# Kernel optimization log

Measured on AMD Instinct MI355X. Metric: run time of the kernel, lower is better.

The kernel has to match this reference:

```python
import jax, jax.numpy as jnp
import numpy as np
from jax import lax

# dims (see shape_source)
B, C, H, W = 2, 128, 48, 48
HEADS = 4
G = 4                 # offset_groups = heads
DH = C // HEADS       # 32, dim_head
DF = 4                # downsample_factor
OKS = 6               # offset_kernel_size
PAD = (OKS - DF) // 2 # 1
OFFSET_SCALE = 4.0
CPB_DIM = C // 4      # 32
OD = C // G           # offset_dims = 32


def setup_inputs() -> dict:
    key = jax.random.key(0)
    ks = jax.random.split(key, 12)
    rn = lambda k, shape, s=0.05: jax.random.normal(k, shape, dtype=jnp.float32) * s
    return {
        "x": jax.random.normal(ks[0], (B, C, H, W), dtype=jnp.float32),
        "gamma": jax.random.normal(ks[1], (1,), dtype=jnp.float32),  # nn.Parameter([0.0]); randomized so both paths contribute
        "wq": rn(ks[2], (G, DH, C // G)),    # grouped 1x1 conv, groups=G
        "wk": rn(ks[3], (G, DH, C // G)),
        "wv": rn(ks[4], (G, DH, C // G)),
        "wo": rn(ks[5], (C, C)),             # to_out 1x1 conv
        "bo": jnp.zeros((C,), jnp.float32),
        "w_off_dw": rn(ks[6], (OD, 1, OKS, OKS)),  # depthwise conv k=6 s=4 p=1
        "b_off_dw": jnp.zeros((OD,), jnp.float32),
        "w_off_proj": rn(ks[7], (2, OD)),          # 1x1 conv to 2 offset channels, no bias
        "cpb_w0": rn(ks[8], (2, CPB_DIM), 0.5),
        "cpb_b0": jnp.zeros((CPB_DIM,), jnp.float32),
        "cpb_w1": rn(ks[9], (CPB_DIM, CPB_DIM), 0.2),
        "cpb_b1": jnp.zeros((CPB_DIM,), jnp.float32),
        "cpb_w2": rn(ks[10], (CPB_DIM, HEADS // G), 0.2),
        "cpb_b2": jnp.zeros((HEADS // G,), jnp.float32),
    }


def _bilinear_sample(img, px, py):
    """F.grid_sample(mode='bilinear', padding_mode='zeros') on pixel coords.
    img: (N, Cg, Hi, Wi); px, py: (N, Ho, Wo) -> (N, Cg, Ho, Wo)"""
    N, Cg, Hi, Wi = img.shape
    imgf = img.reshape(N, Cg, Hi * Wi)
    x0 = jnp.floor(px)
    y0 = jnp.floor(py)
    wx1 = px - x0
    wy1 = py - y0

    def corner(xc, yc, w):
        valid = (xc >= 0) & (xc <= Wi - 1) & (yc >= 0) & (yc <= Hi - 1)
        xi = jnp.clip(xc, 0, Wi - 1).astype(jnp.int32)
        yi = jnp.clip(yc, 0, Hi - 1).astype(jnp.int32)
        idx = (yi * Wi + xi).reshape(N, -1)
        vals = jnp.take_along_axis(imgf, idx[:, None, :], axis=2)  # (N,Cg,Ho*Wo)
        return vals * (w * valid).reshape(N, 1, -1)

    out = (corner(x0, y0, (1 - wx1) * (1 - wy1))
           + corner(x0 + 1, y0, wx1 * (1 - wy1))
           + corner(x0, y0 + 1, (1 - wx1) * wy1)
           + corner(x0 + 1, y0 + 1, wx1 * wy1))
    return out.reshape(N, Cg, px.shape[1], px.shape[2])


def _forward(x, gamma, wq, wk, wv, wo, bo, w_off_dw, b_off_dw, w_off_proj,
             cpb_w0, cpb_b0, cpb_w1, cpb_b1, cpb_w2, cpb_b2):
    b = x.shape[0]
    scale = DH ** -0.5
    xg = x.reshape(b, G, C // G, H, W)
    # grouped 1x1 conv -> queries (b, G, DH, H, W); channel layout (g d) == (h d) since G==HEADS
    q = jnp.einsum('bgchw,goc->bgohw', xg, wq)
    gq = q.reshape(b * G, DH, H, W)
    # to_offsets: depthwise conv (k=6, s=4, p=1) -> GELU -> 1x1 to 2ch -> tanh -> *offset_scale
    off = lax.conv_general_dilated(gq, w_off_dw, (DF, DF), [(PAD, PAD), (PAD, PAD)],
                                   feature_group_count=OD,
                                   dimension_numbers=('NCHW', 'OIHW', 'NCHW'))
    off = jax.nn.gelu(off + b_off_dw[None, :, None, None], approximate=False)
    off = jnp.tanh(jnp.einsum('bchw,oc->bohw', off, w_off_proj)) * OFFSET_SCALE  # (bG,2,Hd,Wd)
    Hd, Wd = off.shape[-2], off.shape[-1]
    gy, gx = jnp.meshgrid(jnp.arange(Hd, dtype=jnp.float32),
                          jnp.arange(Wd, dtype=jnp.float32), indexing='ij')
    vg0 = gx[None] + off[:, 0]  # channel 0 = x (meshgrid 'xy' in torch code)
    vg1 = gy[None] + off[:, 1]  # channel 1 = y
    vn0 = 2.0 * vg0 / max(Hd - 1, 1) - 1.0  # normalize_grid (H==W so h/w quirk is moot)
    vn1 = 2.0 * vg1 / max(Wd - 1, 1) - 1.0
    # grid_sample align_corners=False unnormalization: pix = ((u+1)*size - 1)/2
    px = ((vn0 + 1.0) * W - 1.0) / 2.0
    py = ((vn1 + 1.0) * H - 1.0) / 2.0
    kv = _bilinear_sample(xg.reshape(b * G, C // G, H, W), px, py)  # (bG, C/G, Hd, Wd)
    kvg = kv.reshape(b, G, C // G, Hd, Wd)
    k = jnp.einsum('bgchw,goc->bgohw', kvg, wk)
    v = jnp.einsum('bgchw,goc->bgohw', kvg, wv)
    i, j = H * W, Hd * Wd
    qh = q.reshape(b, HEADS, DH, i).transpose(0, 1, 3, 2) * scale  # (b,h,i,d)
    kh = k.reshape(b, HEADS, DH, j).transpose(0, 1, 3, 2)
    vh = v.reshape(b, HEADS, DH, j).transpose(0, 1, 3, 2)
    sim = jnp.einsum('bhid,bhjd->bhij', qh, kh)
    # CPB relative position bias
    gyq, gxq = jnp.meshgrid(jnp.arange(H, dtype=jnp.float32),
                            jnp.arange(W, dtype=jnp.float32), indexing='ij')
    qn0 = 2.0 * gxq / max(H - 1, 1) - 1.0
    qn1 = 2.0 * gyq / max(W - 1, 1) - 1.0
    grid_q = jnp.stack([qn0, qn1], -1).reshape(1, i, 1, 2)
    grid_kv = jnp.stack([vn0, vn1], -1).reshape(b * G, 1, j, 2)
    pos = grid_q - grid_kv                       # (bG, i, j, 2)
    bias = jnp.sign(pos) * jnp.log1p(jnp.abs(pos))
    h1 = jax.nn.relu(bias @ cpb_w0 + cpb_b0)
    h2 = jax.nn.relu(h1 @ cpb_w1 + cpb_b1)
    bias = h2 @ cpb_w2 + cpb_b2                  # (bG, i, j, heads//G)
    bias = bias.reshape(b, G, i, j, HEADS // G).transpose(0, 1, 4, 2, 3).reshape(b, HEADS, i, j)
    attn = jax.nn.softmax(sim + bias, axis=-1)
    outh = jnp.einsum('bhij,bhjd->bhid', attn, vh)
    out = outh.transpose(0, 1, 3, 2).reshape(b, C, H, W)  # 'b h (x y) d -> b (h d) x y'
    attention = jnp.einsum('bchw,oc->bohw', out, wo) + bo[None, :, None, None]
    return gamma[0] * attention + x, attention


def reference(x, gamma, wq, wk, wv, wo, bo, w_off_dw, b_off_dw, w_off_proj,
              cpb_w0, cpb_b0, cpb_w1, cpb_b1, cpb_w2, cpb_b2):
    return _forward(x, gamma, wq, wk, wv, wo, bo, w_off_dw, b_off_dw, w_off_proj,
                    cpb_w0, cpb_b0, cpb_w1, cpb_b1, cpb_w2, cpb_b2)
```

## Files before the change

kernel.cpp:

```cpp
#include <hip/hip_runtime.h>
#include <math.h>

#define HWHW 2304
#define JD   144
#define LSP  148

typedef __attribute__((ext_vector_type(8))) short short8;
typedef __attribute__((ext_vector_type(4))) float f32x4;

__device__ inline ushort f2bf(float f) {
  uint u = __float_as_uint(f);
  u += 0x7fffu + ((u >> 16) & 1u);
  return (ushort)(u >> 16);
}
__device__ inline float bf2f(ushort s) { return __uint_as_float((uint)s << 16); }
__device__ inline uint packbf(float hi, float lo) {
  return __builtin_amdgcn_perm(__float_as_uint(hi), __float_as_uint(lo), 0x07060302);
}


__global__ __launch_bounds__(256) void qproj_kernel(
    const float* __restrict__ x, const float* __restrict__ wq,
    ushort* __restrict__ qt) {
  int hw = blockIdx.x * 256 + threadIdx.x;
  int o0 = blockIdx.y * 8, bg = blockIdx.z;
  int b = bg >> 2, g = bg & 3;
  const float* xp = x + (b * 128 + g * 32) * HWHW + hw;
  float xv[32];
#pragma unroll
  for (int c = 0; c < 32; ++c) xv[c] = xp[c * HWHW];
  uint p[4];
#pragma unroll
  for (int oo = 0; oo < 8; oo += 2) {
    const float* w0r = wq + (g * 32 + o0 + oo) * 32;
    const float* w1r = wq + (g * 32 + o0 + oo + 1) * 32;
    float a0 = 0.f, a1 = 0.f;
#pragma unroll
    for (int c = 0; c < 32; ++c) { a0 += w0r[c] * xv[c]; a1 += w1r[c] * xv[c]; }
    p[oo >> 1] = (uint)f2bf(a0) | ((uint)f2bf(a1) << 16);
  }
  *(uint4*)(qt + ((long)bg * HWHW + hw) * 32 + o0) = make_uint4(p[0], p[1], p[2], p[3]);
}

__global__ __launch_bounds__(384) void offset_kv_kernel(
    const ushort* __restrict__ qt, const float* __restrict__ wdw,
    const float* __restrict__ bdw, const float* __restrict__ wproj,
    const float* __restrict__ x, const float* __restrict__ wk,
    const float* __restrict__ wv,
    float* __restrict__ vn0, float* __restrict__ vn1,
    ushort* __restrict__ ktb, ushort* __restrict__ vtb) {
  __shared__ float qs[288][32];
  __shared__ float wdws[36][32];
  __shared__ float wkl[32][33], wvl[32][33];
  __shared__ float kvs[32][13];
  __shared__ float spx[12], spy[12];
  int hd = blockIdx.x, bg = blockIdx.y, b = bg >> 2, g = bg & 3;
  int t = threadIdx.x;
  for (int u = t; u < 4608; u += 384) {
    int r = u >> 4, c2 = u & 15;
    int ry = r / 48, col = r - ry * 48;
    int hy = hd * 4 - 1 + ry;
    uint v = 0;
    if (hy >= 0 && hy < 48)
      v = ((const uint*)qt)[((long)bg * HWHW + hy * 48 + col) * 16 + c2];
    qs[r][c2 * 2] = bf2f((ushort)v);
    qs[r][c2 * 2 + 1] = bf2f((ushort)(v >> 16));
  }
  for (int u = t; u < 1152; u += 384) wdws[u >> 5][u & 31] = wdw[(u & 31) * 36 + (u >> 5)];
  for (int u = t; u < 1024; u += 384) {
    int d = u >> 5, c = u & 31;
    wkl[d][c] = wk[g * 1024 + u];
    wvl[d][c] = wv[g * 1024 + u];
  }
  __syncthreads();
  {
    int wd = t >> 5, c = t & 31;
    float s = 0.f;
#pragma unroll
    for (int ky = 0; ky < 6; ++ky) {
#pragma unroll
      for (int kx = 0; kx < 6; ++kx) {
        int wx = wd * 4 - 1 + kx;
        if (wx >= 0 && wx < 48)
          s += wdws[ky * 6 + kx][c] * qs[ky * 48 + wx][c];
      }
    }
    s += bdw[c];
    s = 0.5f * s * (1.f + erff(s * 0.70710678118654752f));
    float g0 = wproj[c] * s;
    float g1 = wproj[32 + c] * s;
#pragma unroll
    for (int k = 16; k >= 1; k >>= 1) {
      g0 += __shfl_xor(g0, k, 64);
      g1 += __shfl_xor(g1, k, 64);
    }
    if (c == 0) {
      float off0 = tanhf(g0) * 4.f;
      float off1 = tanhf(g1) * 4.f;
      float n0 = 2.f * ((float)wd + off0) / 11.f - 1.f;
      float n1 = 2.f * ((float)hd + off1) / 11.f - 1.f;
      int idx = bg * JD + hd * 12 + wd;
      vn0[idx] = n0;
      vn1[idx] = n1;
      spx[wd] = ((n0 + 1.f) * 48.f - 1.f) * 0.5f;
      spy[wd] = ((n1 + 1.f) * 48.f - 1.f) * 0.5f;
    }
  }
  __syncthreads();
  {
    int j = t >> 5, c = t & 31;
    float fx = spx[j], fy = spy[j];
    float x0 = floorf(fx), y0 = floorf(fy);
    float wx = fx - x0, wy = fy - y0;
    int xi = (int)x0, yi = (int)y0;
    const float* xp = x + (b * 128 + g * 32 + c) * HWHW;
    float v00 = 0.f, v10 = 0.f, v01 = 0.f, v11 = 0.f;
    bool okx0 = (xi >= 0) & (xi < 48), okx1 = (xi + 1 >= 0) & (xi + 1 < 48);
    if (yi >= 0 && yi < 48) {
      if (okx0) v00 = xp[yi * 48 + xi];
      if (okx1) v10 = xp[yi * 48 + xi + 1];
    }
    if (yi + 1 >= 0 && yi + 1 < 48) {
      if (okx0) v01 = xp[(yi + 1) * 48 + xi];
      if (okx1) v11 = xp[(yi + 1) * 48 + xi + 1];
    }
    kvs[c][j] = v00 * (1.f - wx) * (1.f - wy) + v10 * wx * (1.f - wy)
              + v01 * (1.f - wx) * wy + v11 * wx * wy;
  }
  __syncthreads();
  {
    int j = t >> 5, d = t & 31;
    float ak = 0.f, av = 0.f;
#pragma unroll
    for (int c = 0; c < 32; ++c) {
      float val = kvs[c][j];
      ak += wkl[d][c] * val;
      av += wvl[d][c] * val;
    }
    int jg = hd * 12 + j;
    ktb[bg * 4608 + jg * 32 + d] = f2bf(ak);
    vtb[bg * 5120 + d * 160 + jg] = f2bf(av);
  }
  if (hd == 0) {
    for (int u = t; u < 512; u += 384)
      vtb[bg * 5120 + (u >> 4) * 160 + 144 + (u & 15)] = 0;
  }
}

__global__ __launch_bounds__(256) void attn_fused_kernel(
    const ushort* __restrict__ qt, const ushort* __restrict__ ktb,
    const ushort* __restrict__ vtb,
    const float* __restrict__ vn0, const float* __restrict__ vn1,
    const float* __restrict__ w0, const float* __restrict__ b0,
    const float* __restrict__ w1, const float* __restrict__ b1,
    const float* __restrict__ w2, const float* __restrict__ b2,
    ushort* __restrict__ outh) {
  __shared__ __align__(16) char smem[10624];
  float* Ls = (float*)smem;
  float* sv0 = (float*)(smem + 9472);
  float* sv1 = (float*)(smem + 10048);

  int bg = blockIdx.y, b = bg >> 2, g = bg & 3;
  int i0 = blockIdx.x * 16;
  int t = threadIdx.x;
  int w = t >> 6, lane = t & 63;
  int lam = lane & 15, quad = lane >> 4;

  if (t < JD) { sv0[t] = vn0[bg * JD + t]; sv1[t] = vn1[bg * JD + t]; }

  float w00r[8], w01r[8], b0r[8];
#pragma unroll
  for (int j = 0; j < 8; ++j) {
    int k = quad * 8 + j;
    w00r[j] = w0[k]; w01r[j] = w0[32 + k]; b0r[j] = b0[k];
  }
  short8 w1f0, w1f1;
#pragma unroll
  for (int j = 0; j < 8; ++j) {
    int k = quad * 8 + j;
    w1f0[j] = (short)f2bf(w1[k * 32 + lam]);
    w1f1[j] = (short)f2bf(w1[k * 32 + 16 + lam]);
  }
  f32x4 zA, zB;
  float w2r[8];
#pragma unroll
  for (int r = 0; r < 4; ++r) {
    zA[r] = b1[quad * 4 + r];
    zB[r] = b1[16 + quad * 4 + r];
    w2r[r] = w2[quad * 4 + r];
    w2r[4 + r] = w2[16 + quad * 4 + r];
  }
  float b2s = b2[0];

  const float scale = 0.17677669529663687f;
  {
    short8 aq = *(const short8*)(qt + ((long)bg * HWHW + i0 + lam) * 32 + quad * 8);
    const ushort* kb = ktb + bg * 4608;
#pragma unroll 1
    for (int jt = w; jt < 9; jt += 4) {
      short8 bk = *(const short8*)(kb + (jt * 16 + lam) * 32 + quad * 8);
      f32x4 acc = {0.f, 0.f, 0.f, 0.f};
      acc = __builtin_amdgcn_mfma_f32_16x16x32_bf16(aq, bk, acc, 0, 0, 0);
#pragma unroll
      for (int r = 0; r < 4; ++r)
        Ls[(quad * 4 + r) * LSP + jt * 16 + lam] = acc[r] * scale;
    }
  }
  __syncthreads();

#pragma unroll 1
  for (int s = 0; s < 9; ++s) {
    int P = s * 64 + lane;
    int ii = P / 144, jj = P - ii * 144;
    int ig = i0 + w * 4 + ii;
    int iy = ig / 48, ix = ig - iy * 48;
    float p0 = (float)ix * (2.f / 47.f) - 1.f - sv0[jj];
    float p1 = (float)iy * (2.f / 47.f) - 1.f - sv1[jj];
    float s0f = copysignf(__logf(1.f + fabsf(p0)), p0);
    float s1f = copysignf(__logf(1.f + fabsf(p1)), p1);
    float bm[4];
#pragma unroll
    for (int mt = 0; mt < 4; ++mt) {
      float s0 = __shfl(s0f, mt * 16 + lam, 64);
      float s1 = __shfl(s1f, mt * 16 + lam, 64);
      float h[8];
#pragma unroll
      for (int j = 0; j < 8; ++j)
        h[j] = fmaxf(fmaf(s0, w00r[j], fmaf(s1, w01r[j], b0r[j])), 0.f);
      union { uint u[4]; short8 s8; } cvt;
#pragma unroll
      for (int j = 0; j < 4; ++j) cvt.u[j] = packbf(h[2 * j + 1], h[2 * j]);
      f32x4 dA = __builtin_amdgcn_mfma_f32_16x16x32_bf16(w1f0, cvt.s8, zA, 0, 0, 0);
      f32x4 dB = __builtin_amdgcn_mfma_f32_16x16x32_bf16(w1f1, cvt.s8, zB, 0, 0, 0);
      float acc = 0.f;
#pragma unroll
      for (int r = 0; r < 4; ++r) {
        acc = fmaf(fmaxf(dA[r], 0.f), w2r[r], acc);
        acc = fmaf(fmaxf(dB[r], 0.f), w2r[4 + r], acc);
      }
      acc += __shfl_xor(acc, 16, 64);
      acc += __shfl_xor(acc, 32, 64);
      bm[mt] = acc;
    }
    float biasv = (quad == 0 ? bm[0] : quad == 1 ? bm[1] : quad == 2 ? bm[2] : bm[3]) + b2s;
    Ls[(w * 4 + ii) * LSP + jj] += biasv;
  }
  __syncthreads();

#pragma unroll 1
  for (int rr = 0; rr < 4; ++rr) {
    int row = w * 4 + rr;
    const float* Lp = Ls + row * LSP;
    float l0 = Lp[lane], l1 = Lp[64 + lane];
    float l2 = (lane < 16) ? Lp[128 + lane] : -INFINITY;
    float m = fmaxf(fmaxf(l0, l1), l2);
#pragma unroll
    for (int k = 32; k >= 1; k >>= 1) m = fmaxf(m, __shfl_xor(m, k, 64));
    float e0 = __expf(l0 - m), e1 = __expf(l1 - m);
    float e2 = (lane < 16) ? __expf(l2 - m) : 0.f;
    float sum = e0 + e1 + e2;
#pragma unroll
    for (int k = 32; k >= 1; k >>= 1) sum += __shfl_xor(sum, k, 64);
    float inv = 1.f / sum;
    ushort* pb = (ushort*)(Lp + 64);
    pb[lane] = f2bf(e0 * inv);
    pb[64 + lane] = f2bf(e1 * inv);
    if (lane < 32) pb[128 + lane] = (lane < 16) ? f2bf(e2 * inv) : (ushort)0;
  }
  __syncthreads();

  if (w < 2) {
    f32x4 o = {0.f, 0.f, 0.f, 0.f};
    const ushort* pb = (const ushort*)(Ls + lam * LSP + 64);
    const ushort* vb = vtb + bg * 5120 + (w * 16 + lam) * 160;
#pragma unroll
    for (int kb = 0; kb < 5; ++kb) {
      short8 ap = *(const short8*)(pb + kb * 32 + quad * 8);
      short8 bv = *(const short8*)(vb + kb * 32 + quad * 8);
      o = __builtin_amdgcn_mfma_f32_16x16x32_bf16(ap, bv, o, 0, 0, 0);
    }
#pragma unroll
    for (int r = 0; r < 4; ++r) {
      int ig = i0 + quad * 4 + r;
      outh[((long)b * HWHW + ig) * 128 + g * 32 + w * 16 + lam] = f2bf(o[r]);
    }
  }
}

__global__ __launch_bounds__(256) void out_kernel(
    const ushort* __restrict__ outh, const float* __restrict__ wo,
    const float* __restrict__ bo, const float* __restrict__ x,
    const float* __restrict__ gamma, float* __restrict__ out) {
  int b = blockIdx.y;
  int hw0 = blockIdx.x * 16;
  int t = threadIdx.x;
  int w = t >> 6, lane = t & 63, lam = lane & 15, quad = lane >> 4;
  const ushort* abase = outh + ((long)b * HWHW + hw0 + lam) * 128 + quad * 8;
  const float* wb0 = wo + (w * 32 + lam) * 128 + quad * 8;
  const float* wb1 = wo + (w * 32 + 16 + lam) * 128 + quad * 8;
  f32x4 acc0 = {0.f, 0.f, 0.f, 0.f}, acc1 = {0.f, 0.f, 0.f, 0.f};
#pragma unroll
  for (int ks = 0; ks < 4; ++ks) {
    short8 a = *(const short8*)(abase + ks * 32);
    float4 wa = *(const float4*)(wb0 + ks * 32);
    float4 wb = *(const float4*)(wb0 + ks * 32 + 4);
    float4 wc = *(const float4*)(wb1 + ks * 32);
    float4 wd = *(const float4*)(wb1 + ks * 32 + 4);
    union { uint u[4]; short8 s8; } p0, p1;
    p0.u[0] = packbf(wa.y, wa.x); p0.u[1] = packbf(wa.w, wa.z);
    p0.u[2] = packbf(wb.y, wb.x); p0.u[3] = packbf(wb.w, wb.z);
    p1.u[0] = packbf(wc.y, wc.x); p1.u[1] = packbf(wc.w, wc.z);
    p1.u[2] = packbf(wd.y, wd.x); p1.u[3] = packbf(wd.w, wd.z);
    acc0 = __builtin_amdgcn_mfma_f32_16x16x32_bf16(a, p0.s8, acc0, 0, 0, 0);
    acc1 = __builtin_amdgcn_mfma_f32_16x16x32_bf16(a, p1.s8, acc1, 0, 0, 0);
  }
  float gm = gamma[0];
  float* out0 = out;
  float* out1 = out + 2 * 128 * HWHW;
#pragma unroll
  for (int nt = 0; nt < 2; ++nt) {
    f32x4 acc = nt ? acc1 : acc0;
    int oc = w * 32 + nt * 16 + lam;
    float bv = bo[oc];
    long base = ((long)(b * 128 + oc)) * HWHW + hw0 + quad * 4;
    float4 xv = *(const float4*)(x + base);
    float4 a1, a0;
    a1.x = acc[0] + bv; a1.y = acc[1] + bv; a1.z = acc[2] + bv; a1.w = acc[3] + bv;
    a0.x = fmaf(gm, a1.x, xv.x); a0.y = fmaf(gm, a1.y, xv.y);
    a0.z = fmaf(gm, a1.z, xv.z); a0.w = fmaf(gm, a1.w, xv.w);
    *(float4*)(out1 + base) = a1;
    *(float4*)(out0 + base) = a0;
  }
}

extern "C" void kernel_launch(void* const* d_in, const int* in_sizes, int n_in,
                              void* d_out, int out_size, void* d_ws, size_t ws_size,
                              hipStream_t stream) {
  const float* x     = (const float*)d_in[0];
  const float* gamma = (const float*)d_in[1];
  const float* wq    = (const float*)d_in[2];
  const float* wk    = (const float*)d_in[3];
  const float* wv    = (const float*)d_in[4];
  const float* wo    = (const float*)d_in[5];
  const float* bo    = (const float*)d_in[6];
  const float* wdw   = (const float*)d_in[7];
  const float* bdw   = (const float*)d_in[8];
  const float* wproj = (const float*)d_in[9];
  const float* cw0   = (const float*)d_in[10];
  const float* cb0   = (const float*)d_in[11];
  const float* cw1   = (const float*)d_in[12];
  const float* cb1   = (const float*)d_in[13];
  const float* cw2   = (const float*)d_in[14];
  const float* cb2   = (const float*)d_in[15];
  char* wsb = (char*)d_ws;
  ushort* qt  = (ushort*)wsb;
  float* vn0  = (float*)(wsb + 1179648);
  float* vn1  = (float*)(wsb + 1184256);
  ushort* ktb = (ushort*)(wsb + 1188864);
  ushort* vtb = (ushort*)(wsb + 1262592);
  ushort* outh = (ushort*)(wsb + 1344512);
  float* out  = (float*)d_out;

  qproj_kernel<<<dim3(9, 4, 8), 256, 0, stream>>>(x, wq, qt);
  offset_kv_kernel<<<dim3(12, 8), 384, 0, stream>>>(qt, wdw, bdw, wproj, x, wk, wv,
                                                    vn0, vn1, ktb, vtb);
  attn_fused_kernel<<<dim3(144, 8), 256, 0, stream>>>(qt, ktb, vtb, vn0, vn1,
                                                      cw0, cb0, cw1, cb1, cw2, cb2, outh);
  out_kernel<<<dim3(144, 2), 256, 0, stream>>>(outh, wo, bo, x, gamma, out);
}
```

Measured before the change: 135.6 us.

## Fuse Q projection into offset and attention kernels via MFMA recompute

Drops the separate Q-projection kernel and its bf16 workspace buffer. The offset/KV kernel and the attention kernel now each recompute their Q tiles directly from x with bf16 MFMA, writing into shared memory. The attention kernel also loads the V fragments into registers before the first barrier, so those loads are no longer on the tail. This saves one launch and a global write-then-read of Q, at the cost of redundant projection work and bf16 rounding of x inside the offset path.

```diff
diff --git a/kernel.cpp b/kernel.cpp
--- a/kernel.cpp
+++ b/kernel.cpp
@@ -19,52 +19,67 @@
 }
 
 
-__global__ __launch_bounds__(256) void qproj_kernel(
+__global__ __launch_bounds__(384) void offset_kv_kernel(
     const float* __restrict__ x, const float* __restrict__ wq,
-    ushort* __restrict__ qt) {
-  int hw = blockIdx.x * 256 + threadIdx.x;
-  int o0 = blockIdx.y * 8, bg = blockIdx.z;
-  int b = bg >> 2, g = bg & 3;
-  const float* xp = x + (b * 128 + g * 32) * HWHW + hw;
-  float xv[32];
-#pragma unroll
-  for (int c = 0; c < 32; ++c) xv[c] = xp[c * HWHW];
-  uint p[4];
-#pragma unroll
-  for (int oo = 0; oo < 8; oo += 2) {
-    const float* w0r = wq + (g * 32 + o0 + oo) * 32;
-    const float* w1r = wq + (g * 32 + o0 + oo + 1) * 32;
-    float a0 = 0.f, a1 = 0.f;
-#pragma unroll
-    for (int c = 0; c < 32; ++c) { a0 += w0r[c] * xv[c]; a1 += w1r[c] * xv[c]; }
-    p[oo >> 1] = (uint)f2bf(a0) | ((uint)f2bf(a1) << 16);
-  }
-  *(uint4*)(qt + ((long)bg * HWHW + hw) * 32 + o0) = make_uint4(p[0], p[1], p[2], p[3]);
-}
-
-__global__ __launch_bounds__(384) void offset_kv_kernel(
-    const ushort* __restrict__ qt, const float* __restrict__ wdw,
-    const float* __restrict__ bdw, const float* __restrict__ wproj,
-    const float* __restrict__ x, const float* __restrict__ wk,
+    const float* __restrict__ wdw, const float* __restrict__ bdw,
+    const float* __restrict__ wproj, const float* __restrict__ wk,
     const float* __restrict__ wv,
     float* __restrict__ vn0, float* __restrict__ vn1,
     ushort* __restrict__ ktb, ushort* __restrict__ vtb) {
-  __shared__ float qs[288][32];
+  __shared__ float qs[288][33];
   __shared__ float wdws[36][32];
   __shared__ float wkl[32][33], wvl[32][33];
   __shared__ float kvs[32][13];
   __shared__ float spx[12], spy[12];
   int hd = blockIdx.x, bg = blockIdx.y, b = bg >> 2, g = bg & 3;
   int t = threadIdx.x;
-  for (int u = t; u < 4608; u += 384) {
-    int r = u >> 4, c2 = u & 15;
-    int ry = r / 48, col = r - ry * 48;
-    int hy = hd * 4 - 1 + ry;
-    uint v = 0;
-    if (hy >= 0 && hy < 48)
-      v = ((const uint*)qt)[((long)bg * HWHW + hy * 48 + col) * 16 + c2];
-    qs[r][c2 * 2] = bf2f((ushort)v);
-    qs[r][c2 * 2 + 1] = bf2f((ushort)(v >> 16));
+  int w = t >> 6, lane = t & 63, lam = lane & 15, quad = lane >> 4;
+
+  {
+    int hy = hd * 4 - 1 + w;
+    if (hy >= 0 && hy < 48) {
+      const float* wqg = wq + (g * 32) * 32;
+      float4 wa = *(const float4*)(wqg + lam * 32 + quad * 8);
+      float4 wb = *(const float4*)(wqg + lam * 32 + quad * 8 + 4);
+      float4 wc = *(const float4*)(wqg + (16 + lam) * 32 + quad * 8);
+      float4 wd = *(const float4*)(wqg + (16 + lam) * 32 + quad * 8 + 4);
+      union { uint u[4]; short8 s8; } bf0, bf1;
+      bf0.u[0] = packbf(wa.y, wa.x); bf0.u[1] = packbf(wa.w, wa.z);
+      bf0.u[2] = packbf(wb.y, wb.x); bf0.u[3] = packbf(wb.w, wb.z);
+      bf1.u[0] = packbf(wc.y, wc.x); bf1.u[1] = packbf(wc.w, wc.z);
+      bf1.u[2] = packbf(wd.y, wd.x); bf1.u[3] = packbf(wd.w, wd.z);
+      const float* xg = x + (b * 128 + g * 32) * HWHW + hy * 48;
+#pragma unroll
+      for (int tt = 0; tt < 3; ++tt) {
+        int col = tt * 16 + lam;
+        union { uint u[4]; short8 s8; } xa;
+#pragma unroll
+        for (int j = 0; j < 4; ++j) {
+          float x0 = xg[(quad * 8 + 2 * j) * HWHW + col];
+          float x1 = xg[(quad * 8 + 2 * j + 1) * HWHW + col];
+          xa.u[j] = packbf(x1, x0);
+        }
+        f32x4 z = {0.f, 0.f, 0.f, 0.f};
+        f32x4 d0 = __builtin_amdgcn_mfma_f32_16x16x32_bf16(xa.s8, bf0.s8, z, 0, 0, 0);
+        f32x4 d1 = __builtin_amdgcn_mfma_f32_16x16x32_bf16(xa.s8, bf1.s8, z, 0, 0, 0);
+        int p = w * 48 + tt * 16 + quad * 4;
+#pragma unroll
+        for (int r = 0; r < 4; ++r) {
+          qs[p + r][lam] = d0[r];
+          qs[p + r][16 + lam] = d1[r];
+        }
+      }
+    } else {
+#pragma unroll
+      for (int tt = 0; tt < 3; ++tt) {
+        int p = w * 48 + tt * 16 + quad * 4;
+#pragma unroll
+        for (int r = 0; r < 4; ++r) {
+          qs[p + r][lam] = 0.f;
+          qs[p + r][16 + lam] = 0.f;
+        }
+      }
+    }
   }
   for (int u = t; u < 1152; u += 384) wdws[u >> 5][u & 31] = wdw[(u & 31) * 36 + (u >> 5)];
   for (int u = t; u < 1024; u += 384) {
@@ -148,17 +163,18 @@
 }
 
 __global__ __launch_bounds__(256) void attn_fused_kernel(
-    const ushort* __restrict__ qt, const ushort* __restrict__ ktb,
-    const ushort* __restrict__ vtb,
+    const float* __restrict__ x, const float* __restrict__ wq,
+    const ushort* __restrict__ ktb, const ushort* __restrict__ vtb,
     const float* __restrict__ vn0, const float* __restrict__ vn1,
     const float* __restrict__ w0, const float* __restrict__ b0,
     const float* __restrict__ w1, const float* __restrict__ b1,
     const float* __restrict__ w2, const float* __restrict__ b2,
     ushort* __restrict__ outh) {
-  __shared__ __align__(16) char smem[10624];
+  __shared__ __align__(16) char smem[11648];
   float* Ls = (float*)smem;
-  float* sv0 = (float*)(smem + 9472);
-  float* sv1 = (float*)(smem + 10048);
+  ushort* qbf = (ushort*)(smem + 9472);
+  float* sv0 = (float*)(smem + 10496);
+  float* sv1 = (float*)(smem + 11072);
 
   int bg = blockIdx.y, b = bg >> 2, g = bg & 3;
   int i0 = blockIdx.x * 16;
@@ -168,6 +184,34 @@
 
   if (t < JD) { sv0[t] = vn0[bg * JD + t]; sv1[t] = vn1[bg * JD + t]; }
 
+  {
+    const float* wqg = wq + (g * 32) * 32;
+    float4 wa = *(const float4*)(wqg + lam * 32 + quad * 8);
+    float4 wb = *(const float4*)(wqg + lam * 32 + quad * 8 + 4);
+    float4 wc = *(const float4*)(wqg + (16 + lam) * 32 + quad * 8);
+    float4 wd = *(const float4*)(wqg + (16 + lam) * 32 + quad * 8 + 4);
+    union { uint u[4]; short8 s8; } bf0, bf1, xa;
+    bf0.u[0] = packbf(wa.y, wa.x); bf0.u[1] = packbf(wa.w, wa.z);
+    bf0.u[2] = packbf(wb.y, wb.x); bf0.u[3] = packbf(wb.w, wb.z);
+    bf1.u[0] = packbf(wc.y, wc.x); bf1.u[1] = packbf(wc.w, wc.z);
+    bf1.u[2] = packbf(wd.y, wd.x); bf1.u[3] = packbf(wd.w, wd.z);
+    const float* xg = x + (b * 128 + g * 32) * HWHW + i0;
+#pragma unroll
+    for (int j = 0; j < 4; ++j) {
+      float x0 = xg[(quad * 8 + 2 * j) * HWHW + lam];
+      float x1 = xg[(quad * 8 + 2 * j + 1) * HWHW + lam];
+      xa.u[j] = packbf(x1, x0);
+    }
+    f32x4 z = {0.f, 0.f, 0.f, 0.f};
+    f32x4 d0 = __builtin_amdgcn_mfma_f32_16x16x32_bf16(xa.s8, bf0.s8, z, 0, 0, 0);
+    f32x4 d1 = __builtin_amdgcn_mfma_f32_16x16x32_bf16(xa.s8, bf1.s8, z, 0, 0, 0);
+#pragma unroll
+    for (int r = 0; r < 4; ++r) {
+      qbf[(quad * 4 + r) * 32 + lam] = f2bf(d0[r]);
+      qbf[(quad * 4 + r) * 32 + 16 + lam] = f2bf(d1[r]);
+    }
+  }
+
   float w00r[8], w01r[8], b0r[8];
 #pragma unroll
   for (int j = 0; j < 8; ++j) {
@@ -192,9 +236,19 @@
   }
   float b2s = b2[0];
 
+  short8 vf[5];
+  if (w < 2) {
+    const ushort* vb = vtb + bg * 5120 + (w * 16 + lam) * 160;
+#pragma unroll
+    for (int kb = 0; kb < 5; ++kb)
+      vf[kb] = *(const short8*)(vb + kb * 32 + quad * 8);
+  }
+
+  __syncthreads();
+
   const float scale = 0.17677669529663687f;
   {
-    short8 aq = *(const short8*)(qt + ((long)bg * HWHW + i0 + lam) * 32 + quad * 8);
+    short8 aq = *(const short8*)(qbf + lam * 32 + quad * 8);
     const ushort* kb = ktb + bg * 4608;
 #pragma unroll 1
     for (int jt = w; jt < 9; jt += 4) {
@@ -272,12 +326,10 @@
   if (w < 2) {
     f32x4 o = {0.f, 0.f, 0.f, 0.f};
     const ushort* pb = (const ushort*)(Ls + lam * LSP + 64);
-    const ushort* vb = vtb + bg * 5120 + (w * 16 + lam) * 160;
 #pragma unroll
     for (int kb = 0; kb < 5; ++kb) {
       short8 ap = *(const short8*)(pb + kb * 32 + quad * 8);
-      short8 bv = *(const short8*)(vb + kb * 32 + quad * 8);
-      o = __builtin_amdgcn_mfma_f32_16x16x32_bf16(ap, bv, o, 0, 0, 0);
+      o = __builtin_amdgcn_mfma_f32_16x16x32_bf16(ap, vf[kb], o, 0, 0, 0);
     }
 #pragma unroll
     for (int r = 0; r < 4; ++r) {
@@ -353,18 +405,16 @@
   const float* cw2   = (const float*)d_in[14];
   const float* cb2   = (const float*)d_in[15];
   char* wsb = (char*)d_ws;
-  ushort* qt  = (ushort*)wsb;
-  float* vn0  = (float*)(wsb + 1179648);
-  float* vn1  = (float*)(wsb + 1184256);
-  ushort* ktb = (ushort*)(wsb + 1188864);
-  ushort* vtb = (ushort*)(wsb + 1262592);
-  ushort* outh = (ushort*)(wsb + 1344512);
+  float* vn0  = (float*)wsb;
+  float* vn1  = (float*)(wsb + 4608);
+  ushort* ktb = (ushort*)(wsb + 9216);
+  ushort* vtb = (ushort*)(wsb + 82944);
+  ushort* outh = (ushort*)(wsb + 164864);
   float* out  = (float*)d_out;
 
-  qproj_kernel<<<dim3(9, 4, 8), 256, 0, stream>>>(x, wq, qt);
-  offset_kv_kernel<<<dim3(12, 8), 384, 0, stream>>>(qt, wdw, bdw, wproj, x, wk, wv,
+  offset_kv_kernel<<<dim3(12, 8), 384, 0, stream>>>(x, wq, wdw, bdw, wproj, wk, wv,
                                                     vn0, vn1, ktb, vtb);
-  attn_fused_kernel<<<dim3(144, 8), 256, 0, stream>>>(qt, ktb, vtb, vn0, vn1,
+  attn_fused_kernel<<<dim3(144, 8), 256, 0, stream>>>(x, wq, ktb, vtb, vn0, vn1,
                                                       cw0, cb0, cw1, cb1, cw2, cb2, outh);
   out_kernel<<<dim3(144, 2), 256, 0, stream>>>(outh, wo, bo, x, gamma, out);
 }
```

Result: faster. 132.0 us (-2.7%).
